# Performance work log

Hardware: AMD Instinct MI355X
Metric: run time of the kernel (lower is better)

Reference implementation:

```python
import jax, jax.numpy as jnp
import numpy as np

B, N = 4, 8192


def setup_inputs() -> dict:
    key = jax.random.key(0)
    k1, k2, k3 = jax.random.split(key, 3)
    pc_pred = jax.random.normal(k1, (B, N, 3), dtype=jnp.float32)
    pc_target = jax.random.normal(k2, (B, N, 3), dtype=jnp.float32)
    fbpp = jax.random.uniform(k3, (B,), dtype=jnp.float32)
    return {"pc_pred": pc_pred, "pc_target": pc_target, "fbpp": fbpp, "lam": 1}


def _chamfer(x, y):
    # x: (B, N, 3), y: (B, M, 3)
    x2 = jnp.sum(x * x, axis=-1)                     # (B, N)
    y2 = jnp.sum(y * y, axis=-1)                     # (B, M)
    xy = jnp.einsum('bnd,bmd->bnm', x, y)            # (B, N, M)
    d2 = jnp.maximum(x2[:, :, None] + y2[:, None, :] - 2.0 * xy, 0.0)
    cham_x = jnp.mean(jnp.min(d2, axis=2), axis=1)   # (B,) pred -> target
    cham_y = jnp.mean(jnp.min(d2, axis=1), axis=1)   # (B,) target -> pred
    return jnp.mean(cham_x + cham_y)                 # scalar (batch mean)


def reference(pc_pred, pc_target, fbpp, lam):
    d = _chamfer(pc_pred, pc_target)
    r = jnp.mean(fbpp)
    return d + lam * r
```

## Files before the change

### kernel.cpp

```cpp
#include <hip/hip_runtime.h>
#include <math.h>


typedef __attribute__((ext_vector_type(8)))  short  short8;
typedef __attribute__((ext_vector_type(16))) float  f32x16;

#define YS      8
#define RPB     256
#define LTILES  32

#define MFMA2(da, db, A, B0, B1) \
    asm("v_mfma_f32_32x32x16_bf16 %0, %2, %3, 0\n\t" \
        "v_mfma_f32_32x32x16_bf16 %1, %2, %4, 0\n\t" \
        "s_nop 7\n\t" \
        "s_nop 7" \
        : "=&v"(da), "=&v"(db) \
        : "v"(A), "v"(B0), "v"(B1))

static __device__ __forceinline__ float min3f(float a, float b, float c) {
    float d;
    asm("v_min3_f32 %0, %1, %2, %3" : "=v"(d) : "v"(a), "v"(b), "v"(c));
    return d;
}

static inline int roundup_h(int v, int a) { return (v + a - 1) / a * a; }

static __device__ __forceinline__ unsigned short f2bf(float f) {
    union { float f; unsigned int u; } v; v.f = f;
    unsigned int r = v.u + 0x7FFFu + ((v.u >> 16) & 1u);
    return (unsigned short)(r >> 16);
}
static __device__ __forceinline__ float bf2f(unsigned short s) {
    union { unsigned int u; float f; } v; v.u = ((unsigned int)s) << 16;
    return v.f;
}
static __device__ __forceinline__ unsigned int pk2(unsigned short lo,
                                                   unsigned short hi) {
    return (unsigned int)lo | ((unsigned int)hi << 16);
}

static __device__ __forceinline__ float allmin32(float v) {
    union { float f; int i; } u, t;
    u.f = v;
    t.i = __builtin_amdgcn_update_dpp(u.i, u.i, 0xB1, 0xF, 0xF, false);
    u.f = fminf(u.f, t.f);
    t.i = __builtin_amdgcn_update_dpp(u.i, u.i, 0x4E, 0xF, 0xF, false);
    u.f = fminf(u.f, t.f);
    t.i = __builtin_amdgcn_update_dpp(u.i, u.i, 0x124, 0xF, 0xF, false);
    u.f = fminf(u.f, t.f);
    t.i = __builtin_amdgcn_update_dpp(u.i, u.i, 0x128, 0xF, 0xF, false);
    u.f = fminf(u.f, t.f);
    t.i = __builtin_amdgcn_ds_swizzle(u.i, 0x401F);
    u.f = fminf(u.f, t.f);
    return u.f;
}

struct PiecesT {
    unsigned short th[3], tl[3], yh[3], yl[3], n2h, n2l;
};
static __device__ __forceinline__ PiecesT pieces(float x, float y, float z) {
    PiecesT p;
    const float xs[3] = {x, y, z};
    const float n2 = x*x + y*y + z*z;
    #pragma unroll
    for (int c = 0; c < 3; ++c) {
        const float t = -2.0f * xs[c];
        p.th[c] = f2bf(t);      p.tl[c] = f2bf(t - bf2f(p.th[c]));
        p.yh[c] = f2bf(xs[c]);  p.yl[c] = f2bf(xs[c] - bf2f(p.yh[c]));
    }
    p.n2h = f2bf(n2); p.n2l = f2bf(n2 - bf2f(p.n2h));
    return p;
}

__global__ __launch_bounds__(256, 4) void fused_sweep(
    const float* __restrict__ pred, const float* __restrict__ targ,
    int B, int N, int M, int NpadP, int NpadT, int NpadMax,
    float* __restrict__ rowpart)
{
    const int tid  = threadIdx.x;
    const int w    = tid >> 6;
    const int lane = tid & 63;
    const int lc   = lane & 31, h = lane >> 5;

    const int SP = NpadMax / RPB;
    int t = blockIdx.x;
    const int sp  = t % SP;  t /= SP;
    const int js  = t % YS;  t /= YS;
    const int b   = t % B;   t /= B;
    const int dir = t;

    const float* __restrict__ xsrc = (dir == 0) ? pred : targ;
    const float* __restrict__ ysrc = (dir == 0) ? targ : pred;
    const int Nx  = (dir == 0) ? N : M;
    const int My  = (dir == 0) ? M : N;
    const int NpadX = (dir == 0) ? NpadP : NpadT;
    const int NpadY = (dir == 0) ? NpadT : NpadP;
    if (sp * RPB >= NpadX) return;

    const int TM  = NpadY / 32;
    const int nt0 = TM / YS;
    const int t0  = js * nt0;

    __shared__ unsigned short ypack[LTILES * 32 * 16];

    const unsigned short ONE = 0x3F80;
    const int row0 = sp * RPB + w * 64;
    short8 a0, a1;
    #pragma unroll
    for (int s = 0; s < 2; ++s) {
        const int row = min(row0 + s * 32 + lc, Nx - 1);
        const float* sx = xsrc + ((size_t)b * Nx + row) * 3;
        const PiecesT p = pieces(sx[0], sx[1], sx[2]);
        short8 v;
        if (h == 0) {
            v[0]=p.th[0]; v[1]=p.th[1]; v[2]=p.th[2]; v[3]=p.tl[0];
            v[4]=p.tl[1]; v[5]=p.tl[2]; v[6]=p.th[0]; v[7]=p.th[1];
        } else {
            v[0]=p.th[2]; v[1]=p.tl[0]; v[2]=p.tl[1]; v[3]=p.tl[2];
            v[4]=ONE;     v[5]=ONE;     v[6]=p.n2h;   v[7]=p.n2l;
        }
        if (s == 0) a0 = v; else a1 = v;
    }

    f32x16 rm0, rm1;
    #pragma unroll
    for (int r = 0; r < 16; ++r) {
        rm0[r] = __builtin_inff(); rm1[r] = __builtin_inff();
    }

    for (int f0 = 0; f0 < nt0; f0 += LTILES) {
        const int fc = min(LTILES, nt0 - f0);
        __syncthreads();
        for (int i = tid; i < fc * 32; i += 256) {
            const int gi  = min((t0 + f0) * 32 + i, My - 1);
            const float* sy = ysrc + ((size_t)b * My + gi) * 3;
            const PiecesT p = pieces(sy[0], sy[1], sy[2]);
            uint4 blo, bhi;
            blo.x = pk2(p.yh[0], p.yh[1]); blo.y = pk2(p.yh[2], p.yh[0]);
            blo.z = pk2(p.yh[1], p.yh[2]); blo.w = pk2(p.yl[0], p.yl[1]);
            bhi.x = pk2(p.yl[2], p.yl[0]); bhi.y = pk2(p.yl[1], p.yl[2]);
            bhi.z = pk2(p.n2h,  p.n2l);    bhi.w = pk2(ONE,  ONE);
            const int tile = i >> 5, pos = i & 31;
            uint4* base = (uint4*)&ypack[(size_t)tile * 512];
            base[pos]      = blo;
            base[32 + pos] = bhi;
        }
        __syncthreads();

        const unsigned short* lp = ypack + (size_t)lane * 8;
        #pragma unroll 4
        for (int j = 0; j < fc; j += 2) {
            const short8 c0 = *reinterpret_cast<const short8*>(lp + (size_t)j * 512);
            const short8 c1 = (j + 1 < fc)
                ? *reinterpret_cast<const short8*>(lp + (size_t)(j + 1) * 512)
                : c0;
            {
                f32x16 da, db;
                MFMA2(da, db, a0, c0, c1);
                #pragma unroll
                for (int r = 0; r < 16; ++r)
                    rm0[r] = min3f(da[r], db[r], rm0[r]);
            }
            {
                f32x16 da, db;
                MFMA2(da, db, a1, c0, c1);
                #pragma unroll
                for (int r = 0; r < 16; ++r)
                    rm1[r] = min3f(da[r], db[r], rm1[r]);
            }
        }
    }

    const size_t outb = (((size_t)dir * B + b) * YS + js) * (size_t)NpadMax;
    #pragma unroll
    for (int r = 0; r < 16; ++r) {
        const float v0 = allmin32(rm0[r]);
        const float v1 = allmin32(rm1[r]);
        if (lc == 0) {
            const int rr = (r & 3) + 8 * (r >> 2) + 4 * h;
            const int ra = row0 + rr, rb = row0 + 32 + rr;
            if (ra < Nx) rowpart[outb + ra] = v0;
            if (rb < Nx) rowpart[outb + rb] = v1;
        }
    }
}

__global__ __launch_bounds__(256) void combine_kernel(
    const float* __restrict__ rowpart, int B, int N, int M,
    int NpadMax, float invBN, float invBM, float* __restrict__ partial)
{
    const int tid = threadIdx.x;
    const int tot = 2 * B * NpadMax;
    float acc = 0.f;
    for (int idx = blockIdx.x * 256 + tid; idx < tot; idx += gridDim.x * 256) {
        const int row = idx % NpadMax;
        const int rem = idx / NpadMax;
        const int b   = rem % B;
        const int dir = rem / B;
        const int Nx  = (dir == 0) ? N : M;
        if (row >= Nx) continue;
        float m = __builtin_inff();
        #pragma unroll
        for (int js = 0; js < YS; ++js)
            m = fminf(m, rowpart[(((size_t)dir * B + b) * YS + js)
                                 * (size_t)NpadMax + row]);
        acc += fmaxf(m, 0.f) * ((dir == 0) ? invBN : invBM);
    }
    __shared__ float sb[256];
    sb[tid] = acc; __syncthreads();
    for (int off2 = 128; off2 > 0; off2 >>= 1) {
        if (tid < off2) sb[tid] += sb[tid + off2];
        __syncthreads();
    }
    if (tid == 0) partial[blockIdx.x] = sb[0];
}

__global__ void finalize_kernel(const float* __restrict__ partial, int np,
                                const float* __restrict__ fbpp, int Bf,
                                const void* __restrict__ lamp,
                                float* __restrict__ out)
{
    __shared__ float sb[256];
    const int tid = threadIdx.x;
    float acc = 0.f;
    for (int i = tid; i < np; i += 256) acc += partial[i];
    sb[tid] = acc;
    __syncthreads();
    for (int off = 128; off > 0; off >>= 1) {
        if (tid < off) sb[tid] += sb[tid + off];
        __syncthreads();
    }
    if (tid == 0) {
        const int li = *(const int*)lamp;
        const float lam = (li >= -1000000 && li <= 1000000)
                            ? (float)li : *(const float*)lamp;
        float fm = 0.f;
        for (int i = 0; i < Bf; ++i) fm += fbpp[i];
        fm /= (float)Bf;
        out[0] = sb[0] + lam * fm;
    }
}

extern "C" void kernel_launch(void* const* d_in, const int* in_sizes, int n_in,
                              void* d_out, int out_size, void* d_ws, size_t ws_size,
                              hipStream_t stream) {
    const float* pred = (const float*)d_in[0];
    const float* targ = (const float*)d_in[1];
    const float* fbpp = (const float*)d_in[2];
    const void*  lamp = d_in[3];

    const int B = in_sizes[2];
    const int N = in_sizes[0] / (3 * B);
    const int M = in_sizes[1] / (3 * B);
    const int NpadP = roundup_h(N, RPB);
    const int NpadT = roundup_h(M, RPB);
    const int NpadMax = (NpadP > NpadT) ? NpadP : NpadT;

    float* rowpart = (float*)d_ws;
    float* partial = rowpart + (size_t)2 * B * YS * NpadMax;
    (void)ws_size;

    const int SP = NpadMax / RPB;
    const int blocks = 2 * B * YS * SP;
    fused_sweep<<<blocks, 256, 0, stream>>>(
        pred, targ, B, N, M, NpadP, NpadT, NpadMax, rowpart);

    combine_kernel<<<256, 256, 0, stream>>>(
        rowpart, B, N, M, NpadMax,
        1.f / ((float)B * (float)N), 1.f / ((float)B * (float)M), partial);

    finalize_kernel<<<1, 256, 0, stream>>>(partial, 256, fbpp, B, lamp,
                                           (float*)d_out);
}
```

Before: 39.09 us.

## Double per-wave row strips to reuse each LDS target tile across four MFMA fragments

Each wave now holds four 32-row query fragments (128 rows) instead of two, and rows per block double to 512. Every target tile loaded from LDS then feeds four MFMA pairs, which halves LDS reads and target-side bf16 packing per output row. The cost is more accumulator registers, so the occupancy hint drops from 4 to 3 blocks per SIMD. The grid also has half as many blocks, which could leave some CUs with less work to balance.

```diff
diff --git a/kernel.cpp b/kernel.cpp
--- a/kernel.cpp
+++ b/kernel.cpp
@@ -6,7 +6,7 @@
 typedef __attribute__((ext_vector_type(16))) float  f32x16;
 
 #define YS      8
-#define RPB     256
+#define RPB     512
 #define LTILES  32
 
 #define MFMA2(da, db, A, B0, B1) \
@@ -23,6 +23,13 @@
     return d;
 }
 
+#define STRIP(rm, A, c0, c1) do { \
+    f32x16 da, db; \
+    MFMA2(da, db, A, c0, c1); \
+    _Pragma("unroll") \
+    for (int r = 0; r < 16; ++r) rm[r] = min3f(da[r], db[r], rm[r]); \
+} while (0)
+
 static inline int roundup_h(int v, int a) { return (v + a - 1) / a * a; }
 
 static __device__ __forceinline__ unsigned short f2bf(float f) {
@@ -72,7 +79,7 @@
     return p;
 }
 
-__global__ __launch_bounds__(256, 4) void fused_sweep(
+__global__ __launch_bounds__(256, 3) void fused_sweep(
     const float* __restrict__ pred, const float* __restrict__ targ,
     int B, int N, int M, int NpadP, int NpadT, int NpadMax,
     float* __restrict__ rowpart)
@@ -104,10 +111,10 @@
     __shared__ unsigned short ypack[LTILES * 32 * 16];
 
     const unsigned short ONE = 0x3F80;
-    const int row0 = sp * RPB + w * 64;
-    short8 a0, a1;
-    #pragma unroll
-    for (int s = 0; s < 2; ++s) {
+    const int row0 = sp * RPB + w * 128;
+    short8 a0, a1, a2, a3;
+    #pragma unroll
+    for (int s = 0; s < 4; ++s) {
         const int row = min(row0 + s * 32 + lc, Nx - 1);
         const float* sx = xsrc + ((size_t)b * Nx + row) * 3;
         const PiecesT p = pieces(sx[0], sx[1], sx[2]);
@@ -119,13 +126,17 @@
             v[0]=p.th[2]; v[1]=p.tl[0]; v[2]=p.tl[1]; v[3]=p.tl[2];
             v[4]=ONE;     v[5]=ONE;     v[6]=p.n2h;   v[7]=p.n2l;
         }
-        if (s == 0) a0 = v; else a1 = v;
-    }
-
-    f32x16 rm0, rm1;
+        if      (s == 0) a0 = v;
+        else if (s == 1) a1 = v;
+        else if (s == 2) a2 = v;
+        else             a3 = v;
+    }
+
+    f32x16 rm0, rm1, rm2, rm3;
     #pragma unroll
     for (int r = 0; r < 16; ++r) {
         rm0[r] = __builtin_inff(); rm1[r] = __builtin_inff();
+        rm2[r] = __builtin_inff(); rm3[r] = __builtin_inff();
     }
 
     for (int f0 = 0; f0 < nt0; f0 += LTILES) {
@@ -148,26 +159,17 @@
         __syncthreads();
 
         const unsigned short* lp = ypack + (size_t)lane * 8;
-        #pragma unroll 4
+        #pragma unroll 2
         for (int j = 0; j < fc; j += 2) {
-            const short8 c0 = *reinterpret_cast<const short8*>(lp + (size_t)j * 512);
+            const short8 c0 = *reinterpret_cast<const short8*>(
+                lp + (size_t)j * 512);
             const short8 c1 = (j + 1 < fc)
                 ? *reinterpret_cast<const short8*>(lp + (size_t)(j + 1) * 512)
                 : c0;
-            {
-                f32x16 da, db;
-                MFMA2(da, db, a0, c0, c1);
-                #pragma unroll
-                for (int r = 0; r < 16; ++r)
-                    rm0[r] = min3f(da[r], db[r], rm0[r]);
-            }
-            {
-                f32x16 da, db;
-                MFMA2(da, db, a1, c0, c1);
-                #pragma unroll
-                for (int r = 0; r < 16; ++r)
-                    rm1[r] = min3f(da[r], db[r], rm1[r]);
-            }
+            STRIP(rm0, a0, c0, c1);
+            STRIP(rm1, a1, c0, c1);
+            STRIP(rm2, a2, c0, c1);
+            STRIP(rm3, a3, c0, c1);
         }
     }
 
@@ -176,11 +178,15 @@
     for (int r = 0; r < 16; ++r) {
         const float v0 = allmin32(rm0[r]);
         const float v1 = allmin32(rm1[r]);
+        const float v2 = allmin32(rm2[r]);
+        const float v3 = allmin32(rm3[r]);
         if (lc == 0) {
             const int rr = (r & 3) + 8 * (r >> 2) + 4 * h;
-            const int ra = row0 + rr, rb = row0 + 32 + rr;
-            if (ra < Nx) rowpart[outb + ra] = v0;
-            if (rb < Nx) rowpart[outb + rb] = v1;
+            const int r0 = row0 + rr;
+            if (r0 < Nx)      rowpart[outb + r0]      = v0;
+            if (r0 + 32 < Nx) rowpart[outb + r0 + 32] = v1;
+            if (r0 + 64 < Nx) rowpart[outb + r0 + 64] = v2;
+            if (r0 + 96 < Nx) rowpart[outb + r0 + 96] = v3;
         }
     }
 }
```

Result: slower. 41.00 us (+4.9%).
